# Optimization experiments

Measured on AMD Instinct MI355X. Metric: run time of the kernel, lower is better.

## Reference

```python
import jax, jax.numpy as jnp
import numpy as np
import math

N = 3072      # number of graph nodes
D = 256       # in_dim == out_dim
H = 8         # heads
EPS = 1e-5    # LayerNorm eps (torch default)


def _glorot(key, shape):
    fan = shape[-2] + shape[-1]
    std = math.sqrt(6.0 / fan)
    return jax.random.uniform(key, shape, jnp.float32, -std, std)


def layer_norm(x, g, b):
    mu = jnp.mean(x, axis=-1, keepdims=True)
    var = jnp.mean(jnp.square(x - mu), axis=-1, keepdims=True)
    return (x - mu) * jax.lax.rsqrt(var + EPS) * g + b


def setup_inputs() -> dict:
    key = jax.random.key(0)
    ks = jax.random.split(key, 12)
    input_x = jax.random.normal(ks[0], (N, D), jnp.float32)
    # degrees: positive floats in [1, 50)
    deg = 1.0 + 49.0 * jax.random.uniform(ks[1], (N,), jnp.float32)
    WQ = _glorot(ks[2], (H, D, D))
    WK = _glorot(ks[3], (H, D, D))
    WV = _glorot(ks[4], (H, D, D))
    # linears stored as [in, out] (math-equivalent to torch's [out,in] transposed)
    lin_attn_w = _glorot(ks[5], (H * D, D)); lin_attn_b = jnp.zeros((D,), jnp.float32)
    lin_w = _glorot(ks[6], (2 * D, D));       lin_b = jnp.zeros((D,), jnp.float32)
    fnn1_w = _glorot(ks[7], (D, D));          fnn1_b = jnp.zeros((D,), jnp.float32)
    fnn2_w = _glorot(ks[8], (D, D));          fnn2_b = jnp.zeros((D,), jnp.float32)
    ln1_g = jnp.ones((D,), jnp.float32); ln1_b = jnp.zeros((D,), jnp.float32)
    ln2_g = jnp.ones((D,), jnp.float32); ln2_b = jnp.zeros((D,), jnp.float32)
    return dict(input_x=input_x, deg=deg, WQ=WQ, WK=WK, WV=WV,
                lin_attn_w=lin_attn_w, lin_attn_b=lin_attn_b,
                lin_w=lin_w, lin_b=lin_b,
                ln1_g=ln1_g, ln1_b=ln1_b,
                fnn1_w=fnn1_w, fnn1_b=fnn1_b,
                fnn2_w=fnn2_w, fnn2_b=fnn2_b,
                ln2_g=ln2_g, ln2_b=ln2_b)


def reference(input_x, deg, WQ, WK, WV, lin_attn_w, lin_attn_b,
              lin_w, lin_b, ln1_g, ln1_b, fnn1_w, fnn1_b,
              fnn2_w, fnn2_b, ln2_g, ln2_b):
    n = input_x.shape[0]
    # --- multi-head attention over all nodes ---
    Q = jnp.einsum('nd,hde->hne', input_x, WQ)   # [H,N,D]
    K = jnp.einsum('nd,hde->hne', input_x, WK)
    V = jnp.einsum('nd,hde->hne', input_x, WV)
    scores = jnp.einsum('hne,hme->hnm', Q, K)    # [H,N,N]
    # diagonal self-mask: QKT[i] += diag_embed(diag(QKT[i]) - 1e20)
    idx = jnp.arange(n)
    diag_vals = scores[:, idx, idx]
    scores = scores.at[:, idx, idx].add(diag_vals - 1e20)
    attn = jax.nn.softmax(scores / math.sqrt(D), axis=-1)
    attn_x = jnp.einsum('hnm,hme->hne', attn, V)           # [H,N,D]
    attn_cat = jnp.transpose(attn_x, (1, 0, 2)).reshape(n, H * D)
    attn_out = attn_cat @ lin_attn_w + lin_attn_b          # [N,D]
    # --- degree-norm concat + residual + LN ---
    x1 = jnp.concatenate([input_x, attn_out / jnp.sqrt(deg)[:, None]], axis=-1)
    x1 = x1 @ lin_w + lin_b
    x1 = layer_norm(input_x + x1, ln1_g, ln1_b)
    # --- FFN block (dropout inactive at eval) ---
    x2 = jax.nn.relu(x1 @ fnn1_w + fnn1_b)
    x2 = x2 @ fnn2_w + fnn2_b
    return layer_norm(x1 + x2, ln2_g, ln2_b)
```

## Files before the change

kernel.cpp:

```cpp
#include <hip/hip_runtime.h>
#include <hip/hip_bf16.h>
#include <stdint.h>

typedef __bf16 bf16x8_t __attribute__((ext_vector_type(8)));
typedef short  s16x8_t  __attribute__((ext_vector_type(8)));
typedef unsigned short u16x4_t __attribute__((ext_vector_type(4)));
typedef float  f32x4_t __attribute__((ext_vector_type(4)));

#define NTOK 3072
#define NHEAD 8
#define NSPLIT 4

__device__ __forceinline__ unsigned short f2bf(float f) {
  union { float f; uint32_t u; } v; v.f = f;
  uint32_t r = v.u + 0x7fffu + ((v.u >> 16) & 1u);
  return (unsigned short)(r >> 16);
}
__device__ __forceinline__ float bf2f(unsigned short s) {
  union { uint32_t u; float f; } v; v.u = ((uint32_t)s) << 16;
  return v.f;
}

__device__ __forceinline__ void gload_lds16(const void* g, void* lds) {
  __builtin_amdgcn_global_load_lds(
      (const __attribute__((address_space(1))) uint32_t*)g,
      (__attribute__((address_space(3))) uint32_t*)lds, 16, 0, 0);
}


__global__ void prep_qkv_w(const float* __restrict__ WQ, const float* __restrict__ WK,
                           const float* __restrict__ WV, unsigned short* __restrict__ out) {
  __shared__ float tile[64][65];
  int z = blockIdx.z;
  int op = z >> 3, h = z & 7;
  const float* W = ((op == 0) ? WQ : (op == 1) ? WK : WV) + (size_t)h * 65536;
  int t = threadIdx.x;
  int tr = t >> 4, tc4 = (t & 15) * 4;
  int d0 = blockIdx.y * 64, e0 = blockIdx.x * 64;
#pragma unroll
  for (int i = 0; i < 4; ++i) {
    int d = i * 16 + tr;
    f32x4_t v = *(const f32x4_t*)(W + (size_t)(d0 + d) * 256 + e0 + tc4);
    tile[d][tc4] = v[0]; tile[d][tc4 + 1] = v[1]; tile[d][tc4 + 2] = v[2]; tile[d][tc4 + 3] = v[3];
  }
  __syncthreads();
#pragma unroll
  for (int i = 0; i < 4; ++i) {
    int e = i * 16 + tr;
    u16x4_t o;
#pragma unroll
    for (int j = 0; j < 4; ++j) o[j] = f2bf(tile[tc4 + j][e]);
    *(u16x4_t*)(out + ((size_t)(z * 256 + e0 + e)) * 256 + d0 + tc4) = o;
  }
}

__global__ void prep_T(const float* __restrict__ W, unsigned short* __restrict__ out,
                       int Din, int Dout) {
  __shared__ float tile[64][65];
  int t = threadIdx.x;
  int tr = t >> 4, tc4 = (t & 15) * 4;
  int d0 = blockIdx.y * 64, e0 = blockIdx.x * 64;
#pragma unroll
  for (int i = 0; i < 4; ++i) {
    int d = i * 16 + tr;
    f32x4_t v = *(const f32x4_t*)(W + (size_t)(d0 + d) * Dout + e0 + tc4);
    tile[d][tc4] = v[0]; tile[d][tc4 + 1] = v[1]; tile[d][tc4 + 2] = v[2]; tile[d][tc4 + 3] = v[3];
  }
  __syncthreads();
#pragma unroll
  for (int i = 0; i < 4; ++i) {
    int e = i * 16 + tr;
    u16x4_t o;
#pragma unroll
    for (int j = 0; j < 4; ++j) o[j] = f2bf(tile[tc4 + j][e]);
    *(u16x4_t*)(out + (size_t)(e0 + e) * Din + d0 + tc4) = o;
  }
}

__global__ void prep_x(const float* __restrict__ x, unsigned short* __restrict__ xa) {
  int idx = blockIdx.x * 256 + threadIdx.x;
  int n = idx >> 8, d = idx & 255;
  xa[(size_t)n * 512 + d] = f2bf(x[idx]);
}

template <int BM, int BN>
__global__ __launch_bounds__(256, 2) void gemm_kernel(
    const unsigned short* __restrict__ A, int lda,
    const unsigned short* __restrict__ B, int ldb,
    void* __restrict__ Cout, int ldc, int Klen,
    const float* __restrict__ bias,
    const float* __restrict__ resid, int ldr,
    const float* __restrict__ deg, int flags,
    float* __restrict__ part, long pstride) {
  constexpr int WM = BM / 2, WN = BN / 2, FM = WM / 16, FN = WN / 16;
  __shared__ unsigned short As[BM * 32];
  __shared__ unsigned short Bs[BN * 32];
  const int t = threadIdx.x;
  const int w = t >> 6, l = t & 63;
  const int l15 = l & 15, lhi = l >> 4;
  const int row0 = blockIdx.y * BM, col0 = blockIdx.x * BN;
  const int wr = (w >> 1) * WM, wc = (w & 1) * WN;

  f32x4_t acc[FM][FN];
#pragma unroll
  for (int m = 0; m < FM; ++m)
#pragma unroll
    for (int n = 0; n < FN; ++n) acc[m][n] = (f32x4_t){0.f, 0.f, 0.f, 0.f};

  const int srow = l >> 2;
  const int spc  = (l & 3) * 16;
  const int kofs0 = blockIdx.z * Klen;
  const int nkt = Klen >> 5;
  for (int kt = 0; kt < nkt; ++kt) {
    const int koff = kofs0 + kt * 32;
    __syncthreads();
#pragma unroll
    for (int c = w; c < BM / 16; c += 4) {
      int ar = c * 16 + srow;
      int lcb = spc ^ (((ar >> 1) & 3) << 4);
      gload_lds16(A + (size_t)(row0 + ar) * lda + koff + (lcb >> 1), &As[c * 512]);
    }
#pragma unroll
    for (int c = w; c < BN / 16; c += 4) {
      int br = c * 16 + srow;
      int lcb = spc ^ (((br >> 1) & 3) << 4);
      gload_lds16(B + (size_t)(col0 + br) * ldb + koff + (lcb >> 1), &Bs[c * 512]);
    }
    __syncthreads();
    bf16x8_t af[FM], bfr[FN];
#pragma unroll
    for (int m = 0; m < FM; ++m) {
      int ar = wr + m * 16 + l15;
      af[m] = *(const bf16x8_t*)(&As[(ar * 64 + ((lhi * 16) ^ (((ar >> 1) & 3) << 4))) >> 1]);
    }
#pragma unroll
    for (int n = 0; n < FN; ++n) {
      int br = wc + n * 16 + l15;
      bfr[n] = *(const bf16x8_t*)(&Bs[(br * 64 + ((lhi * 16) ^ (((br >> 1) & 3) << 4))) >> 1]);
    }
#pragma unroll
    for (int m = 0; m < FM; ++m)
#pragma unroll
      for (int n = 0; n < FN; ++n)
        acc[m][n] = __builtin_amdgcn_mfma_f32_16x16x32_bf16(af[m], bfr[n], acc[m][n], 0, 0, 0);
  }

  const bool relu = flags & 1, obf = flags & 2, dsc = flags & 4, ppart = flags & 8;
#pragma unroll
  for (int m = 0; m < FM; ++m) {
#pragma unroll
    for (int r = 0; r < 4; ++r) {
      int grow = row0 + wr + m * 16 + lhi * 4 + r;
      float sc = dsc ? rsqrtf(deg[grow]) : 1.0f;
#pragma unroll
      for (int n = 0; n < FN; ++n) {
        int gcol = col0 + wc + n * 16 + l15;
        float v = acc[m][n][r];
        if (ppart) {
          part[(size_t)blockIdx.z * pstride + (size_t)grow * ldc + gcol] = v;
          continue;
        }
        if (bias) v += bias[gcol];
        v *= sc;
        if (resid) v += resid[(size_t)grow * ldr + gcol];
        if (relu) v = fmaxf(v, 0.f);
        if (obf)
          ((unsigned short*)Cout)[(size_t)grow * ldc + gcol] = f2bf(v);
        else
          ((float*)Cout)[(size_t)grow * ldc + gcol] = v;
      }
    }
  }
}

__global__ void attn_reduce(const float* __restrict__ part, const float* __restrict__ lab,
                            const float* __restrict__ deg, unsigned short* __restrict__ xa) {
  int n = blockIdx.x, d = threadIdx.x;
  float s = 0.f;
#pragma unroll
  for (int z = 0; z < 4; ++z) s += part[((size_t)z * NTOK + n) * 256 + d];
  xa[(size_t)n * 512 + 256 + d] = f2bf((s + lab[d]) * rsqrtf(deg[n]));
}

#define VSW(e) ((((((e) >> 1) & 3) ^ (((e) >> 3) & 3))) << 4)
__global__ __launch_bounds__(256, 2) void flash_kernel(
    const unsigned short* __restrict__ qkv, unsigned short* __restrict__ pO,
    float* __restrict__ ml) {
  __shared__ unsigned short Ks[32 * 256];
  __shared__ unsigned short Vt[256 * 32];
  __shared__ unsigned short Ps[4][16 * 32];
  const int bid = blockIdx.x;
  const int hs = bid % (NHEAD * NSPLIT);
  const int qb = bid / (NHEAD * NSPLIT);
  const int h = hs / NSPLIT;
  const int split = hs % NSPLIT;
  const int q0 = qb * 64;
  const int t = threadIdx.x, w = t >> 6, l = t & 63;
  const int l15 = l & 15, lhi = l >> 4;

  bf16x8_t qf[8];
  {
    const unsigned short* Qb = qkv + (size_t)(q0 + w * 16 + l15) * 6144 + h * 256 + lhi * 8;
#pragma unroll
    for (int kk = 0; kk < 8; ++kk) qf[kk] = *(const bf16x8_t*)(Qb + kk * 32);
  }
  f32x4_t o[16];
#pragma unroll
  for (int et = 0; et < 16; ++et) o[et] = (f32x4_t){0.f, 0.f, 0.f, 0.f};
  float m_run[4] = {-1e30f, -1e30f, -1e30f, -1e30f};
  float l_run[4] = {0.f, 0.f, 0.f, 0.f};

  const int vn0 = (t & 7) * 4;
  const int ve0 = (t >> 3) * 8;

  const int nt0 = split * (96 / NSPLIT), nt1 = nt0 + 96 / NSPLIT;
  for (int nt = nt0; nt < nt1; ++nt) {
    const int kv0 = nt * 32;
    __syncthreads();
    {
      int rh = l >> 5;
      int pc = (l & 31) * 16;
#pragma unroll
      for (int i = 0; i < 4; ++i) {
        int c = w * 4 + i;
        int kr = c * 2 + rh;
        int lcb = pc ^ ((kr & 7) << 4);
        gload_lds16(qkv + (size_t)(kv0 + kr) * 6144 + 2048 + h * 256 + (lcb >> 1), &Ks[c * 512]);
      }
    }
    {
      s16x8_t rv[4];
      const unsigned short* Vg = qkv + (size_t)(kv0 + vn0) * 6144 + 4096 + h * 256 + ve0;
#pragma unroll
      for (int rr = 0; rr < 4; ++rr) rv[rr] = *(const s16x8_t*)(Vg + rr * 6144);
#pragma unroll
      for (int j = 0; j < 8; ++j) {
        int e = ve0 + j;
        uint64_t pk = (uint64_t)(unsigned short)rv[0][j] |
                      ((uint64_t)(unsigned short)rv[1][j] << 16) |
                      ((uint64_t)(unsigned short)rv[2][j] << 32) |
                      ((uint64_t)(unsigned short)rv[3][j] << 48);
        int pb = e * 64 + ((vn0 * 2) ^ VSW(e));
        *(uint64_t*)(&Vt[pb >> 1]) = pk;
      }
    }
    __syncthreads();

    f32x4_t s[2];
#pragma unroll
    for (int ni = 0; ni < 2; ++ni) s[ni] = (f32x4_t){0.f, 0.f, 0.f, 0.f};
#pragma unroll
    for (int kk = 0; kk < 8; ++kk) {
#pragma unroll
      for (int ni = 0; ni < 2; ++ni) {
        int br = ni * 16 + l15;
        bf16x8_t kb = *(const bf16x8_t*)(&Ks[(br * 512 + ((kk * 64 + lhi * 16) ^ ((br & 7) << 4))) >> 1]);
        s[ni] = __builtin_amdgcn_mfma_f32_16x16x32_bf16(qf[kk], kb, s[ni], 0, 0, 0);
      }
    }

    float p[2][4];
    float alpha[4];
#pragma unroll
    for (int r = 0; r < 4; ++r) {
      int grow = q0 + w * 16 + lhi * 4 + r;
      float sv[2];
      float mx = -1e30f;
#pragma unroll
      for (int ni = 0; ni < 2; ++ni) {
        float x = s[ni][r] * 0.0625f;
        if (kv0 + ni * 16 + l15 == grow) x = -1e30f;
        sv[ni] = x;
        mx = fmaxf(mx, x);
      }
#pragma unroll
      for (int msk = 1; msk < 16; msk <<= 1) mx = fmaxf(mx, __shfl_xor(mx, msk));
      float mn = fmaxf(m_run[r], mx);
      alpha[r] = __expf(m_run[r] - mn);
      m_run[r] = mn;
      float ls = 0.f;
#pragma unroll
      for (int ni = 0; ni < 2; ++ni) {
        float pv = __expf(sv[ni] - mn);
        p[ni][r] = pv;
        ls += pv;
      }
#pragma unroll
      for (int msk = 1; msk < 16; msk <<= 1) ls += __shfl_xor(ls, msk);
      l_run[r] = l_run[r] * alpha[r] + ls;
    }
#pragma unroll
    for (int et = 0; et < 16; ++et)
#pragma unroll
      for (int r = 0; r < 4; ++r) o[et][r] *= alpha[r];

    unsigned short* Pw = &Ps[w][0];
#pragma unroll
    for (int ni = 0; ni < 2; ++ni)
#pragma unroll
      for (int r = 0; r < 4; ++r) {
        int prow = lhi * 4 + r;
        int pb = prow * 64 + ((((ni * 16 + l15) * 2)) ^ (((prow >> 1) & 3) << 4));
        Pw[pb >> 1] = f2bf(p[ni][r]);
      }
    bf16x8_t pa = *(const bf16x8_t*)(&Pw[(l15 * 64 + ((lhi * 16) ^ (((l15 >> 1) & 3) << 4))) >> 1]);
#pragma unroll
    for (int et = 0; et < 16; ++et) {
      int er = et * 16 + l15;
      bf16x8_t vb = *(const bf16x8_t*)(&Vt[(er * 64 + ((lhi * 16) ^ VSW(er))) >> 1]);
      o[et] = __builtin_amdgcn_mfma_f32_16x16x32_bf16(pa, vb, o[et], 0, 0, 0);
    }
  }

  const size_t sh = (size_t)(split * NHEAD + h);
#pragma unroll
  for (int et = 0; et < 16; ++et)
#pragma unroll
    for (int r = 0; r < 4; ++r) {
      int grow = q0 + w * 16 + lhi * 4 + r;
      pO[(sh * NTOK + grow) * 256 + et * 16 + l15] = f2bf(o[et][r]);
    }
  if (l15 == 0) {
#pragma unroll
    for (int r = 0; r < 4; ++r) {
      int grow = q0 + w * 16 + lhi * 4 + r;
      ml[(sh * NTOK + grow) * 2] = m_run[r];
      ml[(sh * NTOK + grow) * 2 + 1] = l_run[r];
    }
  }
}

__global__ void flash_combine(const unsigned short* __restrict__ pO,
                              const float* __restrict__ ml,
                              unsigned short* __restrict__ acat) {
  int n = blockIdx.x, t = threadIdx.x;
  int h = t >> 5, e0 = (t & 31) * 8;
  float ms[NSPLIT], ls[NSPLIT];
  float M = -1e30f;
#pragma unroll
  for (int s = 0; s < NSPLIT; ++s) {
    size_t b = ((size_t)(s * NHEAD + h) * NTOK + n) * 2;
    ms[s] = ml[b]; ls[s] = ml[b + 1];
    M = fmaxf(M, ms[s]);
  }
  float den = 0.f;
  float num[8];
#pragma unroll
  for (int j = 0; j < 8; ++j) num[j] = 0.f;
#pragma unroll
  for (int s = 0; s < NSPLIT; ++s) {
    float ws = __expf(ms[s] - M);
    den += ws * ls[s];
    s16x8_t ov = *(const s16x8_t*)(pO + ((size_t)(s * NHEAD + h) * NTOK + n) * 256 + e0);
#pragma unroll
    for (int j = 0; j < 8; ++j) num[j] += ws * bf2f((unsigned short)ov[j]);
  }
  float rden = 1.0f / den;
  s16x8_t out;
#pragma unroll
  for (int j = 0; j < 8; ++j) out[j] = (short)f2bf(num[j] * rden);
  *(s16x8_t*)(acat + (size_t)n * 2048 + h * 256 + e0) = out;
}

__global__ void ln_kernel(const float* __restrict__ u, const float* __restrict__ g,
                          const float* __restrict__ b, float* __restrict__ outf,
                          unsigned short* __restrict__ outb) {
  int row = blockIdx.x * 4 + (threadIdx.x >> 6);
  int l = threadIdx.x & 63;
  const float* ur = u + (size_t)row * 256;
  f32x4_t v = *(const f32x4_t*)(ur + l * 4);
  float s = v[0] + v[1] + v[2] + v[3];
#pragma unroll
  for (int m = 1; m < 64; m <<= 1) s += __shfl_xor(s, m);
  float mu = s * (1.0f / 256.0f);
  f32x4_t d;
  float vs = 0.f;
#pragma unroll
  for (int i = 0; i < 4; ++i) { d[i] = v[i] - mu; vs += d[i] * d[i]; }
#pragma unroll
  for (int m = 1; m < 64; m <<= 1) vs += __shfl_xor(vs, m);
  float rstd = rsqrtf(vs * (1.0f / 256.0f) + 1e-5f);
  f32x4_t gg = *(const f32x4_t*)(g + l * 4);
  f32x4_t bb = *(const f32x4_t*)(b + l * 4);
#pragma unroll
  for (int i = 0; i < 4; ++i) {
    float o = d[i] * rstd * gg[i] + bb[i];
    if (outf) outf[(size_t)row * 256 + l * 4 + i] = o;
    if (outb) outb[(size_t)row * 256 + l * 4 + i] = f2bf(o);
  }
}

extern "C" void kernel_launch(void* const* d_in, const int* in_sizes, int n_in,
                              void* d_out, int out_size, void* d_ws, size_t ws_size,
                              hipStream_t stream) {
  const float* x    = (const float*)d_in[0];
  const float* deg  = (const float*)d_in[1];
  const float* WQ   = (const float*)d_in[2];
  const float* WK   = (const float*)d_in[3];
  const float* WV   = (const float*)d_in[4];
  const float* law  = (const float*)d_in[5];
  const float* lab  = (const float*)d_in[6];
  const float* lw   = (const float*)d_in[7];
  const float* lb   = (const float*)d_in[8];
  const float* ln1g = (const float*)d_in[9];
  const float* ln1b = (const float*)d_in[10];
  const float* f1w  = (const float*)d_in[11];
  const float* f1b  = (const float*)d_in[12];
  const float* f2w  = (const float*)d_in[13];
  const float* f2b  = (const float*)d_in[14];
  const float* ln2g = (const float*)d_in[15];
  const float* ln2b = (const float*)d_in[16];

  char* ws = (char*)d_ws;
  size_t off = 0;
  auto alloc = [&](size_t bytes) {
    void* p = ws + off;
    off += (bytes + 255) & ~(size_t)255;
    return p;
  };
  unsigned short* qkvwT = (unsigned short*)alloc((size_t)6144 * 256 * 2);
  unsigned short* lawT  = (unsigned short*)alloc((size_t)256 * 2048 * 2);
  unsigned short* lwT   = (unsigned short*)alloc((size_t)256 * 512 * 2);
  unsigned short* f1T   = (unsigned short*)alloc((size_t)256 * 256 * 2);
  unsigned short* f2T   = (unsigned short*)alloc((size_t)256 * 256 * 2);
  unsigned short* xa    = (unsigned short*)alloc((size_t)NTOK * 512 * 2);
  unsigned short* qkv   = (unsigned short*)alloc((size_t)NTOK * 6144 * 2);
  unsigned short* acat  = (unsigned short*)alloc((size_t)NTOK * 2048 * 2);
  unsigned short* pO    = (unsigned short*)alloc((size_t)NSPLIT * NHEAD * NTOK * 256 * 2);
  float*          mlp   = (float*)alloc((size_t)NSPLIT * NHEAD * NTOK * 2 * 4);
  float*          apart = (float*)alloc((size_t)4 * NTOK * 256 * 4);
  float*          u1    = (float*)alloc((size_t)NTOK * 256 * 4);
  float*          x1f   = (float*)alloc((size_t)NTOK * 256 * 4);
  unsigned short* x1b   = (unsigned short*)alloc((size_t)NTOK * 256 * 2);
  unsigned short* tb    = (unsigned short*)alloc((size_t)NTOK * 256 * 2);
  float*          u2    = (float*)alloc((size_t)NTOK * 256 * 4);

  prep_qkv_w<<<dim3(4, 4, 24), 256, 0, stream>>>(WQ, WK, WV, qkvwT);
  prep_T<<<dim3(4, 32), 256, 0, stream>>>(law, lawT, 2048, 256);
  prep_T<<<dim3(4, 8), 256, 0, stream>>>(lw, lwT, 512, 256);
  prep_T<<<dim3(4, 4), 256, 0, stream>>>(f1w, f1T, 256, 256);
  prep_T<<<dim3(4, 4), 256, 0, stream>>>(f2w, f2T, 256, 256);
  prep_x<<<NTOK, 256, 0, stream>>>(x, xa);

  gemm_kernel<128, 128><<<dim3(48, 24), 256, 0, stream>>>(
      xa, 512, qkvwT, 256, qkv, 6144, 256, nullptr, nullptr, 0, nullptr, 2, nullptr, 0);

  flash_kernel<<<NTOK / 64 * NHEAD * NSPLIT, 256, 0, stream>>>(qkv, pO, mlp);
  flash_combine<<<NTOK, 256, 0, stream>>>(pO, mlp, acat);

  gemm_kernel<64, 64><<<dim3(4, 48, 4), 256, 0, stream>>>(
      acat, 2048, lawT, 2048, nullptr, 256, 512, nullptr, nullptr, 0, nullptr, 8,
      apart, (long)NTOK * 256);
  attn_reduce<<<NTOK, 256, 0, stream>>>(apart, lab, deg, xa);

  gemm_kernel<64, 64><<<dim3(4, 48), 256, 0, stream>>>(
      xa, 512, lwT, 512, u1, 256, 512, lb, x, 256, nullptr, 0, nullptr, 0);
  ln_kernel<<<NTOK / 4, 256, 0, stream>>>(u1, ln1g, ln1b, x1f, x1b);

  gemm_kernel<64, 64><<<dim3(4, 48), 256, 0, stream>>>(
      x1b, 256, f1T, 256, tb, 256, 256, f1b, nullptr, 0, nullptr, 1 | 2, nullptr, 0);
  gemm_kernel<64, 64><<<dim3(4, 48), 256, 0, stream>>>(
      tb, 256, f2T, 256, u2, 256, 256, f2b, x1f, 256, nullptr, 0, nullptr, 0);
  ln_kernel<<<NTOK / 4, 256, 0, stream>>>(u2, ln2g, ln2b, (float*)d_out, nullptr);
}
```

Before: 399.5 us.

## Double-buffer K/V tiles in flash kernel and merge prep kernels into one

The flash attention kernel now double-buffers K and V in LDS. It issues the next tile's global loads (K via direct-to-LDS, V into registers) before computing on the current tile, and packs V after the PV MFMAs, so one barrier per iteration replaces two. s_setprio is raised around the MFMA blocks. Separately, the six weight/input prep launches are merged into a single kernel to cut launch overhead. The cost is doubled LDS use for K/V, which may reduce occupancy, plus higher register pressure from holding the prefetched V.

```diff
diff --git a/kernel.cpp b/kernel.cpp
--- a/kernel.cpp
+++ b/kernel.cpp
@@ -27,20 +27,59 @@
       (__attribute__((address_space(3))) uint32_t*)lds, 16, 0, 0);
 }
 
-
-__global__ void prep_qkv_w(const float* __restrict__ WQ, const float* __restrict__ WK,
-                           const float* __restrict__ WV, unsigned short* __restrict__ out) {
+__global__ void prep_all(const float* __restrict__ WQ, const float* __restrict__ WK,
+                         const float* __restrict__ WV, const float* __restrict__ law,
+                         const float* __restrict__ lw, const float* __restrict__ f1w,
+                         const float* __restrict__ f2w, const float* __restrict__ x,
+                         unsigned short* __restrict__ qkvwT, unsigned short* __restrict__ lawT,
+                         unsigned short* __restrict__ lwT, unsigned short* __restrict__ f1T,
+                         unsigned short* __restrict__ f2T, unsigned short* __restrict__ xa) {
   __shared__ float tile[64][65];
-  int z = blockIdx.z;
-  int op = z >> 3, h = z & 7;
-  const float* W = ((op == 0) ? WQ : (op == 1) ? WK : WV) + (size_t)h * 65536;
-  int t = threadIdx.x;
+  const int id = blockIdx.x;
+  const int t = threadIdx.x;
+  if (id >= 576) {
+    int n0 = (id - 576) * 64;
+    int col = (t & 63) * 4;
+#pragma unroll
+    for (int i = 0; i < 16; ++i) {
+      int n = n0 + i * 4 + (t >> 6);
+      f32x4_t v = *(const f32x4_t*)(x + (size_t)n * 256 + col);
+      u16x4_t o;
+#pragma unroll
+      for (int j = 0; j < 4; ++j) o[j] = f2bf(v[j]);
+      *(u16x4_t*)(xa + (size_t)n * 512 + col) = o;
+    }
+    return;
+  }
+  const float* src; unsigned short* dst; int sld, dld, d0, e0;
+  if (id < 384) {
+    int z = id >> 4, tl = id & 15;
+    int op = z >> 3, hh = z & 7;
+    src = ((op == 0) ? WQ : (op == 1) ? WK : WV) + (size_t)hh * 65536;
+    dst = qkvwT + (size_t)z * 65536;
+    sld = 256; dld = 256; d0 = (tl >> 2) * 64; e0 = (tl & 3) * 64;
+  } else if (id < 512) {
+    int tl = id - 384;
+    src = law; dst = lawT; sld = 256; dld = 2048;
+    d0 = (tl >> 2) * 64; e0 = (tl & 3) * 64;
+  } else if (id < 544) {
+    int tl = id - 512;
+    src = lw; dst = lwT; sld = 256; dld = 512;
+    d0 = (tl >> 2) * 64; e0 = (tl & 3) * 64;
+  } else if (id < 560) {
+    int tl = id - 544;
+    src = f1w; dst = f1T; sld = 256; dld = 256;
+    d0 = (tl >> 2) * 64; e0 = (tl & 3) * 64;
+  } else {
+    int tl = id - 560;
+    src = f2w; dst = f2T; sld = 256; dld = 256;
+    d0 = (tl >> 2) * 64; e0 = (tl & 3) * 64;
+  }
   int tr = t >> 4, tc4 = (t & 15) * 4;
-  int d0 = blockIdx.y * 64, e0 = blockIdx.x * 64;
 #pragma unroll
   for (int i = 0; i < 4; ++i) {
     int d = i * 16 + tr;
-    f32x4_t v = *(const f32x4_t*)(W + (size_t)(d0 + d) * 256 + e0 + tc4);
+    f32x4_t v = *(const f32x4_t*)(src + (size_t)(d0 + d) * sld + e0 + tc4);
     tile[d][tc4] = v[0]; tile[d][tc4 + 1] = v[1]; tile[d][tc4 + 2] = v[2]; tile[d][tc4 + 3] = v[3];
   }
   __syncthreads();
@@ -50,37 +89,8 @@
     u16x4_t o;
 #pragma unroll
     for (int j = 0; j < 4; ++j) o[j] = f2bf(tile[tc4 + j][e]);
-    *(u16x4_t*)(out + ((size_t)(z * 256 + e0 + e)) * 256 + d0 + tc4) = o;
-  }
-}
-
-__global__ void prep_T(const float* __restrict__ W, unsigned short* __restrict__ out,
-                       int Din, int Dout) {
-  __shared__ float tile[64][65];
-  int t = threadIdx.x;
-  int tr = t >> 4, tc4 = (t & 15) * 4;
-  int d0 = blockIdx.y * 64, e0 = blockIdx.x * 64;
-#pragma unroll
-  for (int i = 0; i < 4; ++i) {
-    int d = i * 16 + tr;
-    f32x4_t v = *(const f32x4_t*)(W + (size_t)(d0 + d) * Dout + e0 + tc4);
-    tile[d][tc4] = v[0]; tile[d][tc4 + 1] = v[1]; tile[d][tc4 + 2] = v[2]; tile[d][tc4 + 3] = v[3];
-  }
-  __syncthreads();
-#pragma unroll
-  for (int i = 0; i < 4; ++i) {
-    int e = i * 16 + tr;
-    u16x4_t o;
-#pragma unroll
-    for (int j = 0; j < 4; ++j) o[j] = f2bf(tile[tc4 + j][e]);
-    *(u16x4_t*)(out + (size_t)(e0 + e) * Din + d0 + tc4) = o;
-  }
-}
-
-__global__ void prep_x(const float* __restrict__ x, unsigned short* __restrict__ xa) {
-  int idx = blockIdx.x * 256 + threadIdx.x;
-  int n = idx >> 8, d = idx & 255;
-  xa[(size_t)n * 512 + d] = f2bf(x[idx]);
+    *(u16x4_t*)(dst + (size_t)(e0 + e) * dld + d0 + tc4) = o;
+  }
 }
 
 template <int BM, int BN>
@@ -186,8 +196,8 @@
 __global__ __launch_bounds__(256, 2) void flash_kernel(
     const unsigned short* __restrict__ qkv, unsigned short* __restrict__ pO,
     float* __restrict__ ml) {
-  __shared__ unsigned short Ks[32 * 256];
-  __shared__ unsigned short Vt[256 * 32];
+  __shared__ unsigned short Ks[2][32 * 256];
+  __shared__ unsigned short Vt[2][256 * 32];
   __shared__ unsigned short Ps[4][16 * 32];
   const int bid = blockIdx.x;
   const int hs = bid % (NHEAD * NSPLIT);
@@ -198,6 +208,39 @@
   const int t = threadIdx.x, w = t >> 6, l = t & 63;
   const int l15 = l & 15, lhi = l >> 4;
 
+  const int vn0 = (t & 7) * 4;
+  const int ve0 = (t >> 3) * 8;
+
+  auto issueV = [&](int kv0, s16x8_t rv[4]) {
+    const unsigned short* Vg = qkv + (size_t)(kv0 + vn0) * 6144 + 4096 + h * 256 + ve0;
+#pragma unroll
+    for (int rr = 0; rr < 4; ++rr) rv[rr] = *(const s16x8_t*)(Vg + rr * 6144);
+  };
+  auto issueK = [&](int kv0, int buf) {
+    int rh = l >> 5;
+    int pc = (l & 31) * 16;
+#pragma unroll
+    for (int i = 0; i < 4; ++i) {
+      int c = w * 4 + i;
+      int kr = c * 2 + rh;
+      int lcb = pc ^ ((kr & 7) << 4);
+      gload_lds16(qkv + (size_t)(kv0 + kr) * 6144 + 2048 + h * 256 + (lcb >> 1),
+                  &Ks[buf][c * 512]);
+    }
+  };
+  auto packV = [&](s16x8_t rv[4], int buf) {
+#pragma unroll
+    for (int j = 0; j < 8; ++j) {
+      int e = ve0 + j;
+      uint64_t pk = (uint64_t)(unsigned short)rv[0][j] |
+                    ((uint64_t)(unsigned short)rv[1][j] << 16) |
+                    ((uint64_t)(unsigned short)rv[2][j] << 32) |
+                    ((uint64_t)(unsigned short)rv[3][j] << 48);
+      int pb = e * 64 + ((vn0 * 2) ^ VSW(e));
+      *(uint64_t*)(&Vt[buf][pb >> 1]) = pk;
+    }
+  };
+
   bf16x8_t qf[8];
   {
     const unsigned short* Qb = qkv + (size_t)(q0 + w * 16 + l15) * 6144 + h * 256 + lhi * 8;
@@ -210,54 +253,40 @@
   float m_run[4] = {-1e30f, -1e30f, -1e30f, -1e30f};
   float l_run[4] = {0.f, 0.f, 0.f, 0.f};
 
-  const int vn0 = (t & 7) * 4;
-  const int ve0 = (t >> 3) * 8;
-
   const int nt0 = split * (96 / NSPLIT), nt1 = nt0 + 96 / NSPLIT;
+
+  {
+    s16x8_t rva[4];
+    issueV(nt0 * 32, rva);
+    issueK(nt0 * 32, 0);
+    packV(rva, 0);
+  }
+  __syncthreads();
+
   for (int nt = nt0; nt < nt1; ++nt) {
+    const int c = (nt - nt0) & 1;
     const int kv0 = nt * 32;
-    __syncthreads();
-    {
-      int rh = l >> 5;
-      int pc = (l & 31) * 16;
-#pragma unroll
-      for (int i = 0; i < 4; ++i) {
-        int c = w * 4 + i;
-        int kr = c * 2 + rh;
-        int lcb = pc ^ ((kr & 7) << 4);
-        gload_lds16(qkv + (size_t)(kv0 + kr) * 6144 + 2048 + h * 256 + (lcb >> 1), &Ks[c * 512]);
-      }
-    }
-    {
-      s16x8_t rv[4];
-      const unsigned short* Vg = qkv + (size_t)(kv0 + vn0) * 6144 + 4096 + h * 256 + ve0;
-#pragma unroll
-      for (int rr = 0; rr < 4; ++rr) rv[rr] = *(const s16x8_t*)(Vg + rr * 6144);
-#pragma unroll
-      for (int j = 0; j < 8; ++j) {
-        int e = ve0 + j;
-        uint64_t pk = (uint64_t)(unsigned short)rv[0][j] |
-                      ((uint64_t)(unsigned short)rv[1][j] << 16) |
-                      ((uint64_t)(unsigned short)rv[2][j] << 32) |
-                      ((uint64_t)(unsigned short)rv[3][j] << 48);
-        int pb = e * 64 + ((vn0 * 2) ^ VSW(e));
-        *(uint64_t*)(&Vt[pb >> 1]) = pk;
-      }
-    }
-    __syncthreads();
+    const bool have_nxt = (nt + 1 < nt1);
+    s16x8_t rvb[4];
+    if (have_nxt) {
+      issueV(kv0 + 32, rvb);
+      issueK(kv0 + 32, c ^ 1);
+    }
 
     f32x4_t s[2];
 #pragma unroll
     for (int ni = 0; ni < 2; ++ni) s[ni] = (f32x4_t){0.f, 0.f, 0.f, 0.f};
+    __builtin_amdgcn_s_setprio(1);
 #pragma unroll
     for (int kk = 0; kk < 8; ++kk) {
 #pragma unroll
       for (int ni = 0; ni < 2; ++ni) {
         int br = ni * 16 + l15;
-        bf16x8_t kb = *(const bf16x8_t*)(&Ks[(br * 512 + ((kk * 64 + lhi * 16) ^ ((br & 7) << 4))) >> 1]);
+        bf16x8_t kb = *(const bf16x8_t*)(&Ks[c][(br * 512 + ((kk * 64 + lhi * 16) ^ ((br & 7) << 4))) >> 1]);
         s[ni] = __builtin_amdgcn_mfma_f32_16x16x32_bf16(qf[kk], kb, s[ni], 0, 0, 0);
       }
     }
+    __builtin_amdgcn_s_setprio(0);
 
     float p[2][4];
     float alpha[4];
@@ -304,12 +333,17 @@
         Pw[pb >> 1] = f2bf(p[ni][r]);
       }
     bf16x8_t pa = *(const bf16x8_t*)(&Pw[(l15 * 64 + ((lhi * 16) ^ (((l15 >> 1) & 3) << 4))) >> 1]);
+    __builtin_amdgcn_s_setprio(1);
 #pragma unroll
     for (int et = 0; et < 16; ++et) {
       int er = et * 16 + l15;
-      bf16x8_t vb = *(const bf16x8_t*)(&Vt[(er * 64 + ((lhi * 16) ^ VSW(er))) >> 1]);
+      bf16x8_t vb = *(const bf16x8_t*)(&Vt[c][(er * 64 + ((lhi * 16) ^ VSW(er))) >> 1]);
       o[et] = __builtin_amdgcn_mfma_f32_16x16x32_bf16(pa, vb, o[et], 0, 0, 0);
     }
+    __builtin_amdgcn_s_setprio(0);
+
+    if (have_nxt) packV(rvb, c ^ 1);
+    __syncthreads();
   }
 
   const size_t sh = (size_t)(split * NHEAD + h);
@@ -435,12 +469,8 @@
   unsigned short* tb    = (unsigned short*)alloc((size_t)NTOK * 256 * 2);
   float*          u2    = (float*)alloc((size_t)NTOK * 256 * 4);
 
-  prep_qkv_w<<<dim3(4, 4, 24), 256, 0, stream>>>(WQ, WK, WV, qkvwT);
-  prep_T<<<dim3(4, 32), 256, 0, stream>>>(law, lawT, 2048, 256);
-  prep_T<<<dim3(4, 8), 256, 0, stream>>>(lw, lwT, 512, 256);
-  prep_T<<<dim3(4, 4), 256, 0, stream>>>(f1w, f1T, 256, 256);
-  prep_T<<<dim3(4, 4), 256, 0, stream>>>(f2w, f2T, 256, 256);
-  prep_x<<<NTOK, 256, 0, stream>>>(x, xa);
+  prep_all<<<624, 256, 0, stream>>>(WQ, WK, WV, law, lw, f1w, f2w, x,
+                                    qkvwT, lawT, lwT, f1T, f2T, xa);
 
   gemm_kernel<128, 128><<<dim3(48, 24), 256, 0, stream>>>(
       xa, 512, qkvwT, 256, qkv, 6144, 256, nullptr, nullptr, 0, nullptr, 2, nullptr, 0);
```

New measurement: 393.2 us. Within noise of the previous version (-1.6%).
